# Optimization experiments

Hardware: AMD Instinct MI355X
Metric: run time of the kernel (lower is better)

The kernel has to match this reference:

```python
import jax, jax.numpy as jnp
import numpy as np

MAX_IT = 20
LAMBDA_ROF = 7.0
SIGMA = 1.0 / (7.0 * 0.01)
TAU = 0.01
THETA = 0.5
M, N = 4096, 4096


def _forward_weighted_gradient(x, w):
    # x: [1, M, N], w: [2, M, N] -> [2, M, N]
    x0 = x[0]
    gx = jnp.pad(x0[:, 1:] - x0[:, :-1], ((0, 0), (0, 1)))  # last col stays 0
    gy = jnp.pad(x0[1:, :] - x0[:-1, :], ((0, 1), (0, 0)))  # last row stays 0
    return jnp.stack([gx, gy]) * w


def _backward_weighted_divergence(y, w):
    # y, w: [2, M, N] -> [1, M, N]
    yw = w * y
    h, v = yw[0], yw[1]
    d_h = jnp.concatenate([h[:, :1], h[:, 1:-1] - h[:, :-2], -h[:, -2:-1]], axis=1)
    d_v = jnp.concatenate([v[:1, :], v[1:-1, :] - v[:-2, :], -v[-2:-1, :]], axis=0)
    return (d_h + d_v)[None]


def setup_inputs() -> dict:
    key = jax.random.key(0)
    k1, k2, k3 = jax.random.split(key, 3)
    img_obs = jax.random.uniform(k1, (1, M, N), dtype=jnp.float32)
    w = jax.random.uniform(k2, (2, M, N), dtype=jnp.float32)
    y0 = jax.random.uniform(k3, (2, M, N), dtype=jnp.float32)
    return {"img_obs": img_obs, "w": w, "y0": y0}


def reference(img_obs, w, y0):
    denom = 1.0 + LAMBDA_ROF * TAU

    def body(carry, _):
        x, x_tilde, y = carry
        # dual update + L-inf ball projection (prox == clip to [-1, 1])
        y = jnp.clip(y + SIGMA * _forward_weighted_gradient(x_tilde, w), -1.0, 1.0)
        x_old = x
        # primal update
        x = (x + TAU * _backward_weighted_divergence(y, w)
             + LAMBDA_ROF * TAU * img_obs) / denom
        # over-relaxation
        x_tilde = x + THETA * (x - x_old)
        return (x, x_tilde, y), None

    (x, x_tilde, y), _ = jax.lax.scan(body, (img_obs, img_obs, y0), None, length=MAX_IT)
    return x_tilde
```

## Files before the change

### kernel.cpp

```cpp
#include <hip/hip_runtime.h>


#define MM 4096
#define NN 4096
static constexpr size_t PP = (size_t)MM * NN;

static constexpr float SIGMA_F  = 14.285714285714286f;
static constexpr float TAU_F    = 0.01f;
static constexpr float THETA_F  = 0.5f;
static constexpr float LT_F     = 0.07f;
static constexpr float INV_DEN  = 1.0f / 1.07f;

typedef _Float16 h16;
typedef __attribute__((ext_vector_type(8))) _Float16 h16x8;
typedef __attribute__((ext_vector_type(4))) float f32x4;

#define TIR 16
#define TIC 112
#define RRW 20
#define LSW 144

__device__ __forceinline__ float clip1(float v) {
    return fminf(1.0f, fmaxf(-1.0f, v));
}

template<bool H>
__device__ __forceinline__ void gld8(const void* __restrict__ p, long idx, bool ok, float* o) {
    if (!ok) {
        #pragma unroll
        for (int e = 0; e < 8; ++e) o[e] = 0.f;
        return;
    }
    if constexpr (H) {
        h16x8 v = *reinterpret_cast<const h16x8*>(reinterpret_cast<const h16*>(p) + idx);
        #pragma unroll
        for (int e = 0; e < 8; ++e) o[e] = (float)v[e];
    } else {
        const float* q = reinterpret_cast<const float*>(p) + idx;
        f32x4 a = *reinterpret_cast<const f32x4*>(q);
        f32x4 b = *reinterpret_cast<const f32x4*>(q + 4);
        o[0]=a.x;o[1]=a.y;o[2]=a.z;o[3]=a.w;o[4]=b.x;o[5]=b.y;o[6]=b.z;o[7]=b.w;
    }
}

__device__ __forceinline__ void lds8h(const h16* p, float* o) {
    h16x8 v = *reinterpret_cast<const h16x8*>(p);
    #pragma unroll
    for (int e = 0; e < 8; ++e) o[e] = (float)v[e];
}
__device__ __forceinline__ void lds8f(const float* p, float* o) {
    f32x4 a = *reinterpret_cast<const f32x4*>(p);
    f32x4 b = *reinterpret_cast<const f32x4*>(p + 4);
    o[0]=a.x;o[1]=a.y;o[2]=a.z;o[3]=a.w;o[4]=b.x;o[5]=b.y;o[6]=b.z;o[7]=b.w;
}

template<int MODE, bool WH, bool IH>
__global__ __launch_bounds__(320, 4)
void pd2(const h16* __restrict__ xprev, const h16* __restrict__ xcur,
         const void* __restrict__ yin, const void* __restrict__ w,
         const void* __restrict__ img,
         h16* __restrict__ xo1, h16* __restrict__ xo2, h16* __restrict__ yo,
         h16* __restrict__ w_h, h16* __restrict__ img_h,
         float* __restrict__ out)
{
    constexpr bool FIRST = (MODE == 0);
    constexpr bool LAST  = (MODE == 2);
    constexpr bool WRH = (!FIRST) && WH;
    constexpr bool IRH = (!FIRST) && IH;

    __shared__ float sXT[RRW][LSW];
    __shared__ h16   sY0[RRW][LSW];
    __shared__ h16   sY1[RRW][LSW];
    __shared__ h16   sW0[RRW][LSW];
    __shared__ h16   sW1[RRW][LSW];

    const int tid = threadIdx.x;
    const int r = tid >> 4;
    const int s = tid & 15;
    const int l = 8 * s;
    const int L = l + 8;
    const int gi  = blockIdx.y * TIR - 2 + r;
    const int gj0 = blockIdx.x * TIC - 8 + l;
    const long idx = (long)gi * NN + gj0;
    const bool ok = (gi >= 0) & (gi < MM) & (gj0 >= 0) & (gj0 < NN);
    const bool interior = (r >= 2) & (r <= 17) & (s >= 1) & (s <= 14) & (gj0 < NN);
    const bool notbot = gi < MM - 1;

    float xcv[8], y0v[8], y1v[8], w0v[8], w1v[8], gim[8], xtv[8];

    if constexpr (FIRST) {
        gld8<false>(img, idx, ok, gim);
        gld8<false>(yin, idx, ok, y0v);
        gld8<false>(yin, (long)PP + idx, ok, y1v);
        gld8<false>(w, idx, ok, w0v);
        gld8<false>(w, (long)PP + idx, ok, w1v);
        #pragma unroll
        for (int e = 0; e < 8; ++e) { xcv[e] = gim[e]; xtv[e] = gim[e]; }
    } else {
        float xpv[8];
        gld8<true>(xprev, idx, ok, xpv);
        gld8<true>(xcur,  idx, ok, xcv);
        gld8<IRH>(img, idx, ok, gim);
        gld8<true>(yin, idx, ok, y0v);
        gld8<true>(yin, (long)PP + idx, ok, y1v);
        gld8<WRH>(w, idx, ok, w0v);
        gld8<WRH>(w, (long)PP + idx, ok, w1v);
        #pragma unroll
        for (int e = 0; e < 8; ++e) xtv[e] = fmaf(THETA_F, xcv[e] - xpv[e], xcv[e]);
    }

    #pragma unroll
    for (int e = 0; e < 8; ++e) sXT[r][L + e] = xtv[e];
    {
        h16x8 t0, t1;
        #pragma unroll
        for (int e = 0; e < 8; ++e) { t0[e] = (h16)w0v[e]; t1[e] = (h16)w1v[e]; }
        *reinterpret_cast<h16x8*>(&sW0[r][L]) = t0;
        *reinterpret_cast<h16x8*>(&sW1[r][L]) = t1;
        if constexpr (FIRST && WH) {
            if (interior) {
                *reinterpret_cast<h16x8*>(&w_h[idx]) = t0;
                *reinterpret_cast<h16x8*>(&w_h[PP + idx]) = t1;
            }
        }
    }
    if constexpr (FIRST && IH) {
        if (interior) {
            h16x8 tg;
            #pragma unroll
            for (int e = 0; e < 8; ++e) tg[e] = (h16)gim[e];
            *reinterpret_cast<h16x8*>(&img_h[idx]) = tg;
        }
    }
    if (s == 0) {
        #pragma unroll
        for (int e = 0; e < 8; ++e) { sY0[r][e] = (h16)0.f; sW0[r][e] = (h16)0.f; }
    }
    if (s == 15) {
        #pragma unroll
        for (int e = 0; e < 8; ++e) sXT[r][136 + e] = 0.f;
    }
    __syncthreads();

    if (r <= 18) {
        float xtD[8];
        const float xtR = sXT[r][L + 8];
        lds8f(&sXT[r + 1][L], xtD);
        h16x8 t0, t1;
        #pragma unroll
        for (int e = 0; e < 8; ++e) {
            const float xr = (e < 7) ? xtv[e + 1] : xtR;
            const float gx = (gj0 + e < NN - 1) ? (xr - xtv[e]) : 0.f;
            const float gy = notbot ? (xtD[e] - xtv[e]) : 0.f;
            t0[e] = (h16)clip1(fmaf(SIGMA_F * gx, w0v[e], y0v[e]));
            t1[e] = (h16)clip1(fmaf(SIGMA_F * gy, w1v[e], y1v[e]));
            y0v[e] = (float)t0[e];
            y1v[e] = (float)t1[e];
        }
        *reinterpret_cast<h16x8*>(&sY0[r][L]) = t0;
        *reinterpret_cast<h16x8*>(&sY1[r][L]) = t1;
    }
    __syncthreads();

    if (r >= 1 && r <= 18) {
        const float y0L = (float)sY0[r][L - 1];
        const float w0L = (float)sW0[r][L - 1];
        float y1U[8], w1U[8];
        lds8h(&sY1[r - 1][L], y1U);
        lds8h(&sW1[r - 1][L], w1U);
        float hh[8];
        #pragma unroll
        for (int e = 0; e < 8; ++e)
            hh[e] = (gj0 + e < NN - 1) ? w0v[e] * y0v[e] : 0.f;
        float dh[8];
        dh[0] = hh[0] - w0L * y0L;
        #pragma unroll
        for (int e = 1; e < 8; ++e) dh[e] = hh[e] - hh[e - 1];
        h16x8 xh;
        #pragma unroll
        for (int e = 0; e < 8; ++e) {
            const float vC = notbot ? w1v[e] * y1v[e] : 0.f;
            const float vU = w1U[e] * y1U[e];
            const float xv = (xcv[e] + TAU_F * (dh[e] + vC - vU) + LT_F * gim[e]) * INV_DEN;
            const h16 hx = (h16)xv;
            const float xvh = (float)hx;
            xh[e] = hx;
            xtv[e] = fmaf(THETA_F, xvh - xcv[e], xvh);
            xcv[e] = xvh;
        }
        #pragma unroll
        for (int e = 0; e < 8; ++e) sXT[r][L + e] = xtv[e];
        if constexpr (!LAST) {
            if (interior) *reinterpret_cast<h16x8*>(&xo1[idx]) = xh;
        }
    }
    __syncthreads();

    if (r >= 1 && r <= 17) {
        float xtD[8];
        const float xtR = sXT[r][L + 8];
        lds8f(&sXT[r + 1][L], xtD);
        h16x8 t0, t1;
        #pragma unroll
        for (int e = 0; e < 8; ++e) {
            const float xr = (e < 7) ? xtv[e + 1] : xtR;
            const float gx = (gj0 + e < NN - 1) ? (xr - xtv[e]) : 0.f;
            const float gy = notbot ? (xtD[e] - xtv[e]) : 0.f;
            t0[e] = (h16)clip1(fmaf(SIGMA_F * gx, w0v[e], y0v[e]));
            t1[e] = (h16)clip1(fmaf(SIGMA_F * gy, w1v[e], y1v[e]));
            y0v[e] = (float)t0[e];
            y1v[e] = (float)t1[e];
        }
        *reinterpret_cast<h16x8*>(&sY0[r][L]) = t0;
        *reinterpret_cast<h16x8*>(&sY1[r][L]) = t1;
        if constexpr (!LAST) {
            if (interior) {
                *reinterpret_cast<h16x8*>(&yo[idx]) = t0;
                *reinterpret_cast<h16x8*>(&yo[PP + idx]) = t1;
            }
        }
    }
    __syncthreads();

    if (interior) {
        const float y0L = (float)sY0[r][L - 1];
        const float w0L = (float)sW0[r][L - 1];
        float y1U[8], w1U[8];
        lds8h(&sY1[r - 1][L], y1U);
        lds8h(&sW1[r - 1][L], w1U);
        float hh[8];
        #pragma unroll
        for (int e = 0; e < 8; ++e)
            hh[e] = (gj0 + e < NN - 1) ? w0v[e] * y0v[e] : 0.f;
        float dh[8];
        dh[0] = hh[0] - w0L * y0L;
        #pragma unroll
        for (int e = 1; e < 8; ++e) dh[e] = hh[e] - hh[e - 1];
        if constexpr (!LAST) {
            h16x8 xh;
            #pragma unroll
            for (int e = 0; e < 8; ++e) {
                const float vC = notbot ? w1v[e] * y1v[e] : 0.f;
                const float vU = w1U[e] * y1U[e];
                const float xv = (xcv[e] + TAU_F * (dh[e] + vC - vU) + LT_F * gim[e]) * INV_DEN;
                xh[e] = (h16)xv;
            }
            *reinterpret_cast<h16x8*>(&xo2[idx]) = xh;
        } else {
            float o[8];
            #pragma unroll
            for (int e = 0; e < 8; ++e) {
                const float vC = notbot ? w1v[e] * y1v[e] : 0.f;
                const float vU = w1U[e] * y1U[e];
                const float xv = (xcv[e] + TAU_F * (dh[e] + vC - vU) + LT_F * gim[e]) * INV_DEN;
                o[e] = fmaf(THETA_F, xv - xcv[e], xv);
            }
            f32x4 a, b;
            a.x = o[0]; a.y = o[1]; a.z = o[2]; a.w = o[3];
            b.x = o[4]; b.y = o[5]; b.z = o[6]; b.w = o[7];
            *reinterpret_cast<f32x4*>(&out[idx]) = a;
            *reinterpret_cast<f32x4*>(&out[idx + 4]) = b;
        }
    }
}

template<bool WH, bool IH>
static void run_seq(hipStream_t s, const float* img, const float* w, const float* y0,
                    h16* const* xb, h16* yA, h16* yB, h16* w_h, h16* img_h, float* out)
{
    const dim3 grid((NN + TIC - 1) / TIC, MM / TIR);
    const dim3 block(320);
    for (int k = 0; k < 10; ++k) {
        const h16* xp = xb[(2 * k + 3) & 3];
        const h16* xc = xb[(2 * k) & 3];
        h16* xo1 = xb[(2 * k + 1) & 3];
        h16* xo2 = xb[(2 * k + 2) & 3];
        const void* yin = (k == 0) ? (const void*)y0
                                   : ((k & 1) ? (const void*)yA : (const void*)yB);
        h16* yo = (k & 1) ? yB : yA;
        const void* wp = (k == 0) ? (const void*)w
                                  : (WH ? (const void*)w_h : (const void*)w);
        const void* ip = (k == 0) ? (const void*)img
                                  : (IH ? (const void*)img_h : (const void*)img);
        if (k == 0)
            pd2<0, WH, IH><<<grid, block, 0, s>>>(xp, xc, yin, wp, ip, xo1, xo2, yo, w_h, img_h, out);
        else if (k == 9)
            pd2<2, WH, IH><<<grid, block, 0, s>>>(xp, xc, yin, wp, ip, xo1, xo2, yo, w_h, img_h, out);
        else
            pd2<1, WH, IH><<<grid, block, 0, s>>>(xp, xc, yin, wp, ip, xo1, xo2, yo, w_h, img_h, out);
    }
}

extern "C" void kernel_launch(void* const* d_in, const int* in_sizes, int n_in,
                              void* d_out, int out_size, void* d_ws, size_t ws_size,
                              hipStream_t stream) {
    const float* img = (const float*)d_in[0];
    const float* w   = (const float*)d_in[1];
    const float* y0  = (const float*)d_in[2];

    h16* base = (h16*)d_ws;
    h16* xb[4] = { base, base + PP, base + 2 * PP, base + 3 * PP };
    h16* yA = base + 4 * PP;

    const size_t planes = ws_size / (PP * sizeof(h16));
    const bool WH = planes >= 8;
    const bool IH = (planes >= 9) || (planes == 7);
    h16* w_h   = WH ? base + 6 * PP : nullptr;
    h16* img_h = IH ? (WH ? base + 8 * PP : base + 6 * PP) : nullptr;

    h16* yB = (h16*)d_out;
    float* out = (float*)d_out;

    if (WH && IH)      run_seq<true,  true >(stream, img, w, y0, xb, yA, yB, w_h, img_h, out);
    else if (WH)       run_seq<true,  false>(stream, img, w, y0, xb, yA, yB, w_h, img_h, out);
    else if (IH)       run_seq<false, true >(stream, img, w, y0, xb, yA, yB, w_h, img_h, out);
    else               run_seq<false, false>(stream, img, w, y0, xb, yA, yB, w_h, img_h, out);
}
```

Before: 1.535 ms.

## Replace LDS halo exchange with wave shuffles and load upper w1 row from global

Drops the shared-memory copies of y0, w0 and w1. Horizontal neighbours now come from __shfl_up/__shfl_down within the 16-lane row, and the upper-row w1 is read straight from global memory. The shared tiles for sXT and sY1 are narrowed, and the launch bounds are raised from 4 to 8 blocks per SM to get more occupancy. The price is an extra global load per thread and more register pressure under the tighter occupancy bound.

New measurement: 3.401 ms. 122% more time.

```diff
diff --git a/kernel.cpp b/kernel.cpp
--- a/kernel.cpp
+++ b/kernel.cpp
@@ -18,7 +18,8 @@
 #define TIR 16
 #define TIC 112
 #define RRW 20
-#define LSW 144
+#define XTW 132
+#define Y1W 136
 
 __device__ __forceinline__ float clip1(float v) {
     return fminf(1.0f, fmaxf(-1.0f, v));
@@ -43,6 +44,26 @@
     }
 }
 
+template<bool H>
+__device__ __forceinline__ h16x8 gldp8(const void* __restrict__ p, long idx, bool ok) {
+    h16x8 v;
+    if (ok) {
+        if constexpr (H) {
+            v = *reinterpret_cast<const h16x8*>(reinterpret_cast<const h16*>(p) + idx);
+        } else {
+            const float* q = reinterpret_cast<const float*>(p) + idx;
+            f32x4 a = *reinterpret_cast<const f32x4*>(q);
+            f32x4 b = *reinterpret_cast<const f32x4*>(q + 4);
+            v[0]=(h16)a.x; v[1]=(h16)a.y; v[2]=(h16)a.z; v[3]=(h16)a.w;
+            v[4]=(h16)b.x; v[5]=(h16)b.y; v[6]=(h16)b.z; v[7]=(h16)b.w;
+        }
+    } else {
+        #pragma unroll
+        for (int e = 0; e < 8; ++e) v[e] = (h16)0.f;
+    }
+    return v;
+}
+
 __device__ __forceinline__ void lds8h(const h16* p, float* o) {
     h16x8 v = *reinterpret_cast<const h16x8*>(p);
     #pragma unroll
@@ -55,7 +76,7 @@
 }
 
 template<int MODE, bool WH, bool IH>
-__global__ __launch_bounds__(320, 4)
+__global__ __launch_bounds__(320, 8)
 void pd2(const h16* __restrict__ xprev, const h16* __restrict__ xcur,
          const void* __restrict__ yin, const void* __restrict__ w,
          const void* __restrict__ img,
@@ -68,25 +89,24 @@
     constexpr bool WRH = (!FIRST) && WH;
     constexpr bool IRH = (!FIRST) && IH;
 
-    __shared__ float sXT[RRW][LSW];
-    __shared__ h16   sY0[RRW][LSW];
-    __shared__ h16   sY1[RRW][LSW];
-    __shared__ h16   sW0[RRW][LSW];
-    __shared__ h16   sW1[RRW][LSW];
+    __shared__ float sXT[RRW][XTW];
+    __shared__ h16   sY1[RRW][Y1W];
 
     const int tid = threadIdx.x;
     const int r = tid >> 4;
     const int s = tid & 15;
     const int l = 8 * s;
-    const int L = l + 8;
     const int gi  = blockIdx.y * TIR - 2 + r;
     const int gj0 = blockIdx.x * TIC - 8 + l;
     const long idx = (long)gi * NN + gj0;
-    const bool ok = (gi >= 0) & (gi < MM) & (gj0 >= 0) & (gj0 < NN);
+    const bool okc = (gj0 >= 0) & (gj0 < NN);
+    const bool ok  = (gi >= 0) & (gi < MM) & okc;
+    const bool okU = (gi >= 1) & (gi <= MM) & okc;
+    const bool notbot = gi < MM - 1;
     const bool interior = (r >= 2) & (r <= 17) & (s >= 1) & (s <= 14) & (gj0 < NN);
-    const bool notbot = gi < MM - 1;
 
     float xcv[8], y0v[8], y1v[8], w0v[8], w1v[8], gim[8], xtv[8];
+    h16x8 w1Up;
 
     if constexpr (FIRST) {
         gld8<false>(img, idx, ok, gim);
@@ -94,6 +114,7 @@
         gld8<false>(yin, (long)PP + idx, ok, y1v);
         gld8<false>(w, idx, ok, w0v);
         gld8<false>(w, (long)PP + idx, ok, w1v);
+        w1Up = gldp8<false>(w, (long)PP + idx - NN, okU);
         #pragma unroll
         for (int e = 0; e < 8; ++e) { xcv[e] = gim[e]; xtv[e] = gim[e]; }
     } else {
@@ -105,23 +126,21 @@
         gld8<true>(yin, (long)PP + idx, ok, y1v);
         gld8<WRH>(w, idx, ok, w0v);
         gld8<WRH>(w, (long)PP + idx, ok, w1v);
+        w1Up = gldp8<WRH>(w, (long)PP + idx - NN, okU);
         #pragma unroll
         for (int e = 0; e < 8; ++e) xtv[e] = fmaf(THETA_F, xcv[e] - xpv[e], xcv[e]);
     }
 
     #pragma unroll
-    for (int e = 0; e < 8; ++e) sXT[r][L + e] = xtv[e];
-    {
-        h16x8 t0, t1;
-        #pragma unroll
-        for (int e = 0; e < 8; ++e) { t0[e] = (h16)w0v[e]; t1[e] = (h16)w1v[e]; }
-        *reinterpret_cast<h16x8*>(&sW0[r][L]) = t0;
-        *reinterpret_cast<h16x8*>(&sW1[r][L]) = t1;
-        if constexpr (FIRST && WH) {
-            if (interior) {
-                *reinterpret_cast<h16x8*>(&w_h[idx]) = t0;
-                *reinterpret_cast<h16x8*>(&w_h[PP + idx]) = t1;
-            }
+    for (int e = 0; e < 8; ++e) sXT[r][l + e] = xtv[e];
+
+    if constexpr (FIRST && WH) {
+        if (interior) {
+            h16x8 t0, t1;
+            #pragma unroll
+            for (int e = 0; e < 8; ++e) { t0[e] = (h16)w0v[e]; t1[e] = (h16)w1v[e]; }
+            *reinterpret_cast<h16x8*>(&w_h[idx]) = t0;
+            *reinterpret_cast<h16x8*>(&w_h[PP + idx]) = t1;
         }
     }
     if constexpr (FIRST && IH) {
@@ -132,134 +151,129 @@
             *reinterpret_cast<h16x8*>(&img_h[idx]) = tg;
         }
     }
-    if (s == 0) {
-        #pragma unroll
-        for (int e = 0; e < 8; ++e) { sY0[r][e] = (h16)0.f; sW0[r][e] = (h16)0.f; }
-    }
-    if (s == 15) {
-        #pragma unroll
-        for (int e = 0; e < 8; ++e) sXT[r][136 + e] = 0.f;
-    }
+    const float w0Ls = __shfl_up(w0v[7], 1);
     __syncthreads();
 
-    if (r <= 18) {
-        float xtD[8];
-        const float xtR = sXT[r][L + 8];
-        lds8f(&sXT[r + 1][L], xtD);
-        h16x8 t0, t1;
-        #pragma unroll
-        for (int e = 0; e < 8; ++e) {
-            const float xr = (e < 7) ? xtv[e + 1] : xtR;
-            const float gx = (gj0 + e < NN - 1) ? (xr - xtv[e]) : 0.f;
-            const float gy = notbot ? (xtD[e] - xtv[e]) : 0.f;
-            t0[e] = (h16)clip1(fmaf(SIGMA_F * gx, w0v[e], y0v[e]));
-            t1[e] = (h16)clip1(fmaf(SIGMA_F * gy, w1v[e], y1v[e]));
-            y0v[e] = (float)t0[e];
-            y1v[e] = (float)t1[e];
-        }
-        *reinterpret_cast<h16x8*>(&sY0[r][L]) = t0;
-        *reinterpret_cast<h16x8*>(&sY1[r][L]) = t1;
+    {
+        const float xtR = __shfl_down(xtv[0], 1);
+        if (r <= 18) {
+            float xtD[8];
+            lds8f(&sXT[r + 1][l], xtD);
+            h16x8 t1;
+            #pragma unroll
+            for (int e = 0; e < 8; ++e) {
+                const float xr = (e < 7) ? xtv[e + 1] : xtR;
+                const float gx = (gj0 + e < NN - 1) ? (xr - xtv[e]) : 0.f;
+                const float gy = notbot ? (xtD[e] - xtv[e]) : 0.f;
+                const h16 t0 = (h16)clip1(fmaf(SIGMA_F * gx, w0v[e], y0v[e]));
+                t1[e] = (h16)clip1(fmaf(SIGMA_F * gy, w1v[e], y1v[e]));
+                y0v[e] = (float)t0;
+                y1v[e] = (float)t1[e];
+            }
+            *reinterpret_cast<h16x8*>(&sY1[r][l]) = t1;
+        }
     }
     __syncthreads();
 
-    if (r >= 1 && r <= 18) {
-        const float y0L = (float)sY0[r][L - 1];
-        const float w0L = (float)sW0[r][L - 1];
-        float y1U[8], w1U[8];
-        lds8h(&sY1[r - 1][L], y1U);
-        lds8h(&sW1[r - 1][L], w1U);
-        float hh[8];
-        #pragma unroll
-        for (int e = 0; e < 8; ++e)
-            hh[e] = (gj0 + e < NN - 1) ? w0v[e] * y0v[e] : 0.f;
-        float dh[8];
-        dh[0] = hh[0] - w0L * y0L;
-        #pragma unroll
-        for (int e = 1; e < 8; ++e) dh[e] = hh[e] - hh[e - 1];
-        h16x8 xh;
-        #pragma unroll
-        for (int e = 0; e < 8; ++e) {
-            const float vC = notbot ? w1v[e] * y1v[e] : 0.f;
-            const float vU = w1U[e] * y1U[e];
-            const float xv = (xcv[e] + TAU_F * (dh[e] + vC - vU) + LT_F * gim[e]) * INV_DEN;
-            const h16 hx = (h16)xv;
-            const float xvh = (float)hx;
-            xh[e] = hx;
-            xtv[e] = fmaf(THETA_F, xvh - xcv[e], xvh);
-            xcv[e] = xvh;
-        }
-        #pragma unroll
-        for (int e = 0; e < 8; ++e) sXT[r][L + e] = xtv[e];
-        if constexpr (!LAST) {
-            if (interior) *reinterpret_cast<h16x8*>(&xo1[idx]) = xh;
-        }
-    }
-    __syncthreads();
-
-    if (r >= 1 && r <= 17) {
-        float xtD[8];
-        const float xtR = sXT[r][L + 8];
-        lds8f(&sXT[r + 1][L], xtD);
-        h16x8 t0, t1;
-        #pragma unroll
-        for (int e = 0; e < 8; ++e) {
-            const float xr = (e < 7) ? xtv[e + 1] : xtR;
-            const float gx = (gj0 + e < NN - 1) ? (xr - xtv[e]) : 0.f;
-            const float gy = notbot ? (xtD[e] - xtv[e]) : 0.f;
-            t0[e] = (h16)clip1(fmaf(SIGMA_F * gx, w0v[e], y0v[e]));
-            t1[e] = (h16)clip1(fmaf(SIGMA_F * gy, w1v[e], y1v[e]));
-            y0v[e] = (float)t0[e];
-            y1v[e] = (float)t1[e];
-        }
-        *reinterpret_cast<h16x8*>(&sY0[r][L]) = t0;
-        *reinterpret_cast<h16x8*>(&sY1[r][L]) = t1;
-        if constexpr (!LAST) {
-            if (interior) {
-                *reinterpret_cast<h16x8*>(&yo[idx]) = t0;
-                *reinterpret_cast<h16x8*>(&yo[PP + idx]) = t1;
-            }
-        }
-    }
-    __syncthreads();
-
-    if (interior) {
-        const float y0L = (float)sY0[r][L - 1];
-        const float w0L = (float)sW0[r][L - 1];
-        float y1U[8], w1U[8];
-        lds8h(&sY1[r - 1][L], y1U);
-        lds8h(&sW1[r - 1][L], w1U);
-        float hh[8];
-        #pragma unroll
-        for (int e = 0; e < 8; ++e)
-            hh[e] = (gj0 + e < NN - 1) ? w0v[e] * y0v[e] : 0.f;
-        float dh[8];
-        dh[0] = hh[0] - w0L * y0L;
-        #pragma unroll
-        for (int e = 1; e < 8; ++e) dh[e] = hh[e] - hh[e - 1];
-        if constexpr (!LAST) {
+    {
+        const float y0Ls = __shfl_up(y0v[7], 1);
+        if (r >= 1 && r <= 18) {
+            float y1U[8];
+            lds8h(&sY1[r - 1][l], y1U);
+            float hh[8];
+            #pragma unroll
+            for (int e = 0; e < 8; ++e)
+                hh[e] = (gj0 + e < NN - 1) ? w0v[e] * y0v[e] : 0.f;
+            float dh[8];
+            dh[0] = hh[0] - ((s == 0) ? 0.f : w0Ls * y0Ls);
+            #pragma unroll
+            for (int e = 1; e < 8; ++e) dh[e] = hh[e] - hh[e - 1];
             h16x8 xh;
             #pragma unroll
             for (int e = 0; e < 8; ++e) {
                 const float vC = notbot ? w1v[e] * y1v[e] : 0.f;
-                const float vU = w1U[e] * y1U[e];
+                const float vU = (float)w1Up[e] * y1U[e];
                 const float xv = (xcv[e] + TAU_F * (dh[e] + vC - vU) + LT_F * gim[e]) * INV_DEN;
-                xh[e] = (h16)xv;
-            }
-            *reinterpret_cast<h16x8*>(&xo2[idx]) = xh;
-        } else {
-            float o[8];
+                const h16 hx = (h16)xv;
+                const float xvh = (float)hx;
+                xh[e] = hx;
+                xtv[e] = fmaf(THETA_F, xvh - xcv[e], xvh);
+                xcv[e] = xvh;
+            }
+            #pragma unroll
+            for (int e = 0; e < 8; ++e) sXT[r][l + e] = xtv[e];
+            if constexpr (!LAST) {
+                if (interior) *reinterpret_cast<h16x8*>(&xo1[idx]) = xh;
+            }
+        }
+    }
+    __syncthreads();
+
+    {
+        const float xtR = __shfl_down(xtv[0], 1);
+        if (r >= 1 && r <= 17) {
+            float xtD[8];
+            lds8f(&sXT[r + 1][l], xtD);
+            h16x8 t0, t1;
             #pragma unroll
             for (int e = 0; e < 8; ++e) {
-                const float vC = notbot ? w1v[e] * y1v[e] : 0.f;
-                const float vU = w1U[e] * y1U[e];
-                const float xv = (xcv[e] + TAU_F * (dh[e] + vC - vU) + LT_F * gim[e]) * INV_DEN;
-                o[e] = fmaf(THETA_F, xv - xcv[e], xv);
-            }
-            f32x4 a, b;
-            a.x = o[0]; a.y = o[1]; a.z = o[2]; a.w = o[3];
-            b.x = o[4]; b.y = o[5]; b.z = o[6]; b.w = o[7];
-            *reinterpret_cast<f32x4*>(&out[idx]) = a;
-            *reinterpret_cast<f32x4*>(&out[idx + 4]) = b;
+                const float xr = (e < 7) ? xtv[e + 1] : xtR;
+                const float gx = (gj0 + e < NN - 1) ? (xr - xtv[e]) : 0.f;
+                const float gy = notbot ? (xtD[e] - xtv[e]) : 0.f;
+                t0[e] = (h16)clip1(fmaf(SIGMA_F * gx, w0v[e], y0v[e]));
+                t1[e] = (h16)clip1(fmaf(SIGMA_F * gy, w1v[e], y1v[e]));
+                y0v[e] = (float)t0[e];
+                y1v[e] = (float)t1[e];
+            }
+            *reinterpret_cast<h16x8*>(&sY1[r][l]) = t1;
+            if constexpr (!LAST) {
+                if (interior) {
+                    *reinterpret_cast<h16x8*>(&yo[idx]) = t0;
+                    *reinterpret_cast<h16x8*>(&yo[PP + idx]) = t1;
+                }
+            }
+        }
+    }
+    __syncthreads();
+
+    {
+        const float y0Ls = __shfl_up(y0v[7], 1);
+        if (interior) {
+            float y1U[8];
+            lds8h(&sY1[r - 1][l], y1U);
+            float hh[8];
+            #pragma unroll
+            for (int e = 0; e < 8; ++e)
+                hh[e] = (gj0 + e < NN - 1) ? w0v[e] * y0v[e] : 0.f;
+            float dh[8];
+            dh[0] = hh[0] - w0Ls * y0Ls;
+            #pragma unroll
+            for (int e = 1; e < 8; ++e) dh[e] = hh[e] - hh[e - 1];
+            if constexpr (!LAST) {
+                h16x8 xh;
+                #pragma unroll
+                for (int e = 0; e < 8; ++e) {
+                    const float vC = notbot ? w1v[e] * y1v[e] : 0.f;
+                    const float vU = (float)w1Up[e] * y1U[e];
+                    const float xv = (xcv[e] + TAU_F * (dh[e] + vC - vU) + LT_F * gim[e]) * INV_DEN;
+                    xh[e] = (h16)xv;
+                }
+                *reinterpret_cast<h16x8*>(&xo2[idx]) = xh;
+            } else {
+                float o[8];
+                #pragma unroll
+                for (int e = 0; e < 8; ++e) {
+                    const float vC = notbot ? w1v[e] * y1v[e] : 0.f;
+                    const float vU = (float)w1Up[e] * y1U[e];
+                    const float xv = (xcv[e] + TAU_F * (dh[e] + vC - vU) + LT_F * gim[e]) * INV_DEN;
+                    o[e] = fmaf(THETA_F, xv - xcv[e], xv);
+                }
+                f32x4 a, b;
+                a.x = o[0]; a.y = o[1]; a.z = o[2]; a.w = o[3];
+                b.x = o[4]; b.y = o[5]; b.z = o[6]; b.w = o[7];
+                *reinterpret_cast<f32x4*>(&out[idx]) = a;
+                *reinterpret_cast<f32x4*>(&out[idx + 4]) = b;
+            }
         }
     }
 }
```
